# Optimization experiments

Hardware: AMD Instinct MI355X
Metric: run time of the kernel (lower is better)

## Reference

```python
import jax, jax.numpy as jnp
import numpy as np

B, S, D, K = 8, 4096, 256, 8192
BETA = 0.25


def setup_inputs() -> dict:
    key = jax.random.key(0)
    k1, k2 = jax.random.split(key)
    return {
        "z": jax.random.normal(k1, (B, S, D), dtype=jnp.float32),
        "embed": jax.random.normal(k2, (K, D), dtype=jnp.float32),
    }


def reference(z, embed):
    # Inference-path VQ-EMA forward (EMA buffer updates are a no-grad side
    # effect only active in training mode; excluded from the pure reference).
    num_codes, dim = embed.shape
    z_flat = z.reshape(-1, dim)                      # [N, D]
    # squared-euclidean distances: ||z||^2 - 2 z.e^T + ||e||^2  -> [N, K]
    dist = ((z_flat * z_flat).sum(1, keepdims=True)
            - 2.0 * (z_flat @ embed.T)
            + (embed * embed).sum(1)[None, :])
    idx = jnp.argmin(dist, axis=1)                   # [N]
    z_q = embed[idx].reshape(z.shape)                # gather instead of onehot @ embed
    # commitment loss: beta * mse(stop_grad(z_q), z)
    loss = BETA * jnp.mean(jnp.square(jax.lax.stop_gradient(z_q) - z))
    # straight-through estimator
    z_q_st = z + jax.lax.stop_gradient(z_q - z)
    # perplexity from code usage histogram (scatter-add instead of onehot.mean)
    counts = jnp.zeros((num_codes,), dtype=z.dtype).at[idx].add(1.0)
    avg_probs = counts / idx.shape[0]
    perplexity = jnp.exp(-jnp.sum(avg_probs * jnp.log(avg_probs + 1e-12)))
    return z_q_st, loss, perplexity, idx.reshape(z.shape[:-1])
```

## Files before the change

kernel.cpp:

```cpp
#include <hip/hip_runtime.h>
#include <stdint.h>
#include <math.h>

#define NROWS 32768
#define DIM   256
#define KCODES 8192
#define BETA  0.25f
#define RSPLIT 16
#define NELEM 8388608
#define TAU 0.09375f

typedef float f32x4 __attribute__((ext_vector_type(4)));
typedef _Float16 v8h __attribute__((ext_vector_type(8)));
typedef unsigned short us4 __attribute__((ext_vector_type(4)));

__device__ inline unsigned int split1(float x) {
    _Float16 hf = (_Float16)x;
    _Float16 lf = (_Float16)(x - (float)hf);
    unsigned int h = __builtin_bit_cast(unsigned short, hf);
    unsigned int l = __builtin_bit_cast(unsigned short, lf);
    return h | (l << 16);
}

__device__ inline void gload_lds16(const void* g, void* l) {
    __builtin_amdgcn_global_load_lds(
        (const __attribute__((address_space(1))) void*)g,
        (__attribute__((address_space(3))) void*)l,
        16, 0, 0);
}

__device__ inline unsigned int fkey(float f) {
    unsigned int b = __float_as_uint(f);
    return (b & 0x80000000u) ? ~b : (b | 0x80000000u);
}

__global__ void prep_all(const float* __restrict__ z,
                         const float* __restrict__ e,
                         unsigned short* __restrict__ zhi,
                         unsigned short* __restrict__ zlo,
                         unsigned short* __restrict__ ehi,
                         unsigned short* __restrict__ elo,
                         float* __restrict__ enrm,
                         float* __restrict__ counts,
                         float* __restrict__ lossAcc,
                         int* __restrict__ flagcnt) {
    if (blockIdx.x < 8192) {
        int t = blockIdx.x * 256 + threadIdx.x;
        float4 v = reinterpret_cast<const float4*>(z)[t];
        unsigned int p0 = split1(v.x);
        unsigned int p1 = split1(v.y);
        unsigned int p2 = split1(v.z);
        unsigned int p3 = split1(v.w);
        us4 h, l;
        h[0] = (unsigned short)p0; l[0] = (unsigned short)(p0 >> 16);
        h[1] = (unsigned short)p1; l[1] = (unsigned short)(p1 >> 16);
        h[2] = (unsigned short)p2; l[2] = (unsigned short)(p2 >> 16);
        h[3] = (unsigned short)p3; l[3] = (unsigned short)(p3 >> 16);
        reinterpret_cast<us4*>(zhi)[t] = h;
        reinterpret_cast<us4*>(zlo)[t] = l;
    } else {
        int row = blockIdx.x - 8192;
        int d = threadIdx.x;
        float x = e[(size_t)row * DIM + d];
        unsigned int p = split1(x);
        ehi[(size_t)row * DIM + d] = (unsigned short)p;
        elo[(size_t)row * DIM + d] = (unsigned short)(p >> 16);
        float sq = x * x;
        #pragma unroll
        for (int off = 32; off; off >>= 1) sq += __shfl_down(sq, off);
        __shared__ float ps[4];
        if ((threadIdx.x & 63) == 0) ps[threadIdx.x >> 6] = sq;
        __syncthreads();
        if (threadIdx.x == 0) {
            enrm[row] = 0.5f * (ps[0] + ps[1] + ps[2] + ps[3]);
            counts[row] = 0.f;
            if (row == 0) { *lossAcc = 0.f; *flagcnt = 0; }
        }
    }
}

__launch_bounds__(512, 2)
__global__ void gemm_hi_fused(const unsigned short* __restrict__ zhi,
                              const unsigned short* __restrict__ ehi,
                              const float* __restrict__ enrm,
                              int* __restrict__ colidx,
                              float* __restrict__ out_idx,
                              int* __restrict__ flagcnt,
                              int* __restrict__ flaglist,
                              unsigned long long* __restrict__ rkey) {
    __shared__ __align__(16) unsigned short Bs[4][128 * 128];
    __shared__ float rvv[4][128];
    __shared__ float rv2s[4][128];
    __shared__ int   rcc[4][128];

    const int tid = threadIdx.x;
    const int w = tid >> 6, l = tid & 63;
    const int lx = l & 15, quad = l >> 4;
    const int wm = w >> 2, wn = w & 3;
    const int arow_base = blockIdx.x * 128;
    const int fr_lx7 = lx & 7;
    const int ecol = wn * 32 + lx;

    const int st_row = w * 4 + (l >> 4);
    const int st_sw = ((l & 15) ^ (st_row & 7)) * 8;

    v8h af[4][8];
    #pragma unroll
    for (int mi = 0; mi < 4; ++mi) {
        const unsigned short* ap =
            zhi + (size_t)(arow_base + wm * 64 + mi * 16 + lx) * DIM + quad * 8;
        #pragma unroll
        for (int ks = 0; ks < 8; ++ks)
            af[mi][ks] = *(const v8h*)(ap + ks * 32);
    }

#define STAGE(BUF, CNT, KB) do {                                              \
        const unsigned short* _s = ehi                                        \
            + (((size_t)(CNT) * 128 + st_row) << 8) + (KB) * 128 + st_sw;     \
        unsigned short* _d = &Bs[BUF][(w * 4) * 128];                         \
        gload_lds16(_s,             _d);                                      \
        gload_lds16(_s + (32 << 8), _d + 32 * 128);                           \
        gload_lds16(_s + (64 << 8), _d + 64 * 128);                           \
        gload_lds16(_s + (96 << 8), _d + 96 * 128);                           \
} while (0)

#define FENCE_MFMA(BUF, BK) do {                                              \
        asm volatile("s_waitcnt vmcnt(14)" ::: "memory");                     \
        __builtin_amdgcn_s_barrier();                                         \
        asm volatile("" ::: "memory");                                        \
        __builtin_amdgcn_s_setprio(1);                                        \
        _Pragma("unroll") for (int kc = 0; kc < 4; ++kc) {                    \
            const int gsw = ((kc * 4 + quad) ^ fr_lx7) * 8;                   \
            v8h b0 = *(const v8h*)&Bs[BUF][(wn * 32 + lx) * 128 + gsw];       \
            v8h b1 = *(const v8h*)&Bs[BUF][(wn * 32 + 16 + lx) * 128 + gsw];  \
            _Pragma("unroll") for (int mi = 0; mi < 4; ++mi) {                \
                acc[mi][0] = __builtin_amdgcn_mfma_f32_16x16x32_f16(          \
                    af[mi][(BK) * 4 + kc], b0, acc[mi][0], 0, 0, 0);          \
                acc[mi][1] = __builtin_amdgcn_mfma_f32_16x16x32_f16(          \
                    af[mi][(BK) * 4 + kc], b1, acc[mi][1], 0, 0, 0);          \
            }                                                                 \
        }                                                                     \
        __builtin_amdgcn_s_setprio(0);                                        \
        asm volatile("" ::: "memory");                                        \
        __builtin_amdgcn_s_barrier();                                         \
} while (0)

#define EPILOGUE(NT) do {                                                     \
        _Pragma("unroll") for (int ni = 0; ni < 2; ++ni) {                    \
            const int col = (NT) * 128 + ecol + ni * 16;                      \
            _Pragma("unroll") for (int mi = 0; mi < 4; ++mi)                  \
                _Pragma("unroll") for (int r = 0; r < 4; ++r) {               \
                    const int s = mi * 4 + r;                                 \
                    const float a = acc[mi][ni][r];                           \
                    const bool gt = a > runm[s];                              \
                    runm2[s] = __builtin_amdgcn_fmed3f(a, runm[s], runm2[s]); \
                    runc[s] = gt ? col : runc[s];                             \
                    runm[s] = fmaxf(runm[s], a);                              \
                }                                                             \
        }                                                                     \
} while (0)

#define STEP_BK0(BUF, NT) do {                                                \
        const float a0 = -esn0, a1 = -esn1;                                   \
        _Pragma("unroll") for (int mi = 0; mi < 4; ++mi) {                    \
            acc[mi][0] = (f32x4){a0, a0, a0, a0};                             \
            acc[mi][1] = (f32x4){a1, a1, a1, a1};                             \
        }                                                                     \
        { const int nn = ((NT) + 1) & 63;                                     \
          esn0 = enrm[nn * 128 + ecol];                                       \
          esn1 = enrm[nn * 128 + ecol + 16]; }                                \
        STAGE((BUF + 3) & 3, ((NT) + 1) & 63, 1);                             \
        FENCE_MFMA(BUF, 0);                                                   \
} while (0)

#define STEP_BK1(BUF, NT) do {                                                \
        STAGE((BUF + 3) & 3, ((NT) + 2) & 63, 0);                             \
        FENCE_MFMA(BUF, 1);                                                   \
        EPILOGUE(NT);                                                         \
} while (0)

    float esn0 = enrm[ecol];
    float esn1 = enrm[ecol + 16];
    STAGE(0, 0, 0); STAGE(1, 0, 1); STAGE(2, 1, 0);

    float runm[16], runm2[16];
    int runc[16];
    #pragma unroll
    for (int s = 0; s < 16; ++s) {
        runm[s] = -3.0e38f; runm2[s] = -3.0e38f; runc[s] = 0x7fffffff;
    }

    f32x4 acc[4][2];
    for (int nt2 = 0; nt2 < 32; ++nt2) {
        const int nt0 = nt2 * 2;
        STEP_BK0(0, nt0);
        STEP_BK1(1, nt0);
        STEP_BK0(2, nt0 + 1);
        STEP_BK1(3, nt0 + 1);
    }
#undef STAGE
#undef FENCE_MFMA
#undef EPILOGUE
#undef STEP_BK0
#undef STEP_BK1

    #pragma unroll
    for (int s = 0; s < 16; ++s) {
        float m1 = runm[s], m2 = runm2[s];
        int c1 = runc[s];
        #pragma unroll
        for (int m = 1; m < 16; m <<= 1) {
            float o1 = __shfl_xor(m1, m);
            int oc = __shfl_xor(c1, m);
            float o2 = __shfl_xor(m2, m);
            float mn = fminf(m1, o1);
            m2 = fmaxf(fmaxf(m2, o2), mn);
            bool take = (o1 > m1) || (o1 == m1 && oc < c1);
            m1 = take ? o1 : m1;
            c1 = take ? oc : c1;
        }
        if (lx == 0) {
            const int rl = wm * 64 + (s >> 2) * 16 + quad * 4 + (s & 3);
            rvv[wn][rl] = m1; rcc[wn][rl] = c1; rv2s[wn][rl] = m2;
        }
    }
    __syncthreads();
    if (tid < 128) {
        float m1 = rvv[0][tid], m2 = rv2s[0][tid];
        int c1 = rcc[0][tid];
        #pragma unroll
        for (int q = 1; q < 4; ++q) {
            float o1 = rvv[q][tid], o2 = rv2s[q][tid];
            int oc = rcc[q][tid];
            float mn = fminf(m1, o1);
            m2 = fmaxf(fmaxf(m2, o2), mn);
            bool take = (o1 > m1) || (o1 == m1 && oc < c1);
            m1 = take ? o1 : m1;
            c1 = take ? oc : c1;
        }
        const float v1 = -m1, v2 = -m2;
        const int row = arow_base + tid;
        out_idx[row] = (float)c1;
        if (v2 - v1 < TAU) {
            int slot = atomicAdd(flagcnt, 1);
            flaglist[slot] = row;
            rkey[slot] = ~0ull;
            colidx[row] = -(slot + 1);
        } else {
            colidx[row] = c1;
        }
    }
}

__launch_bounds__(256, 2)
__global__ void rescue_gemm(const unsigned short* __restrict__ zhi,
                            const unsigned short* __restrict__ zlo,
                            const unsigned short* __restrict__ ehi,
                            const unsigned short* __restrict__ elo,
                            const float* __restrict__ enrm,
                            const int* __restrict__ flagcnt,
                            const int* __restrict__ flaglist,
                            unsigned long long* __restrict__ rkey) {
    __shared__ __align__(16) unsigned short As[128 * 64];
    __shared__ __align__(16) unsigned short Bs[128 * 64];
    __shared__ float rv[2][128];
    __shared__ int   rc[2][128];

    const int count = *flagcnt;
    const int tid = threadIdx.x;
    const int w = tid >> 6, l = tid & 63;
    const int lx = l & 15, quad = l >> 4;
    const int wm = w >> 1, wn = w & 1;
    const int cs = blockIdx.y;
    const int cbase_cs = cs * (KCODES / RSPLIT);

    const int st_row8 = l >> 3;
    const int st_g = (((l & 7) ^ (l >> 3)) * 8);
    const int fr_lx7 = lx & 7;

    for (int tb = blockIdx.x * 128; tb < count; tb += 32 * 128) {
        int arowj[4];
        #pragma unroll
        for (int j = 0; j < 4; ++j) {
            int li = tb + w * 32 + j * 8 + st_row8;
            arowj[j] = (li < count) ? flaglist[li] : 0;
        }

        float runv[16];
        int runc[16];
        #pragma unroll
        for (int s = 0; s < 16; ++s) { runv[s] = 3.0e38f; runc[s] = 0x7fffffff; }

        for (int nt = 0; nt < (KCODES / RSPLIT) / 128; ++nt) {
            const int colbase = cbase_cs + nt * 128;
            f32x4 acc[4][4];
            #pragma unroll
            for (int mi = 0; mi < 4; ++mi)
                #pragma unroll
                for (int ni = 0; ni < 4; ++ni) {
                    f32x4 zz = {0.f, 0.f, 0.f, 0.f};
                    acc[mi][ni] = zz;
                }

            #pragma unroll
            for (int seg = 0; seg < 3; ++seg) {
                const unsigned short* za = (seg == 2) ? zlo : zhi;
                const unsigned short* eb = (seg == 1) ? elo : ehi;
                for (int bk = 0; bk < 4; ++bk) {
                    const int ao = bk * 64;
                    __syncthreads();
                    #pragma unroll
                    for (int j = 0; j < 4; ++j) {
                        const int r = w * 32 + j * 8 + st_row8;
                        gload_lds16(za + (size_t)arowj[j] * DIM + ao + st_g,
                                    &As[(w * 32 + j * 8) * 64]);
                        gload_lds16(eb + (size_t)(colbase + r) * DIM + ao + st_g,
                                    &Bs[(w * 32 + j * 8) * 64]);
                    }
                    __syncthreads();
                    #pragma unroll
                    for (int kc = 0; kc < 2; ++kc) {
                        const int gsw = ((kc * 4 + quad) ^ fr_lx7) * 8;
                        v8h af[4], bfr[4];
                        #pragma unroll
                        for (int mi = 0; mi < 4; ++mi)
                            af[mi] = *(const v8h*)&As[(wm * 64 + mi * 16 + lx) * 64 + gsw];
                        #pragma unroll
                        for (int ni = 0; ni < 4; ++ni)
                            bfr[ni] = *(const v8h*)&Bs[(wn * 64 + ni * 16 + lx) * 64 + gsw];
                        #pragma unroll
                        for (int mi = 0; mi < 4; ++mi)
                            #pragma unroll
                            for (int ni = 0; ni < 4; ++ni)
                                acc[mi][ni] = __builtin_amdgcn_mfma_f32_16x16x32_f16(
                                    af[mi], bfr[ni], acc[mi][ni], 0, 0, 0);
                    }
                }
            }

            #pragma unroll
            for (int ni = 0; ni < 4; ++ni) {
                const int col = colbase + wn * 64 + ni * 16 + lx;
                const float es = enrm[col];
                #pragma unroll
                for (int mi = 0; mi < 4; ++mi)
                    #pragma unroll
                    for (int r = 0; r < 4; ++r) {
                        float sv = es - acc[mi][ni][r];
                        const int s = mi * 4 + r;
                        if (sv < runv[s]) { runv[s] = sv; runc[s] = col; }
                    }
            }
        }

        #pragma unroll
        for (int s = 0; s < 16; ++s) {
            float v = runv[s]; int c = runc[s];
            #pragma unroll
            for (int m = 1; m < 16; m <<= 1) {
                float ov = __shfl_xor(v, m);
                int oc = __shfl_xor(c, m);
                if (ov < v || (ov == v && oc < c)) { v = ov; c = oc; }
            }
            if (lx == 0) {
                const int mi = s >> 2, r = s & 3;
                const int rl = wm * 64 + mi * 16 + quad * 4 + r;
                rv[wn][rl] = v; rc[wn][rl] = c;
            }
        }
        __syncthreads();
        if (tid < 128) {
            float v0 = rv[0][tid]; int c0 = rc[0][tid];
            float v1 = rv[1][tid]; int c1 = rc[1][tid];
            if (v1 < v0 || (v1 == v0 && c1 < c0)) { v0 = v1; c0 = c1; }
            const int li = tb + tid;
            if (li < count) {
                unsigned long long key =
                    ((unsigned long long)fkey(v0) << 32) | (unsigned int)c0;
                atomicMin(&rkey[li], key);
            }
        }
        __syncthreads();
    }
}

__global__ void fused_out(const int* __restrict__ colidx,
                          const unsigned long long* __restrict__ rkey,
                          const float* __restrict__ z,
                          const float* __restrict__ embed,
                          float* __restrict__ out_zq,
                          float* __restrict__ out_idx,
                          float* __restrict__ counts,
                          float* __restrict__ lossAcc) {
    __shared__ int cidx[16];
    const int tid = threadIdx.x;
    if (tid < 16) {
        const int row = blockIdx.x * 16 + tid;
        int c = colidx[row];
        if (c < 0) {
            c = (int)(unsigned int)(rkey[-c - 1] & 0x1FFFull);
            out_idx[row] = (float)c;
        }
        cidx[tid] = c;
        atomicAdd(&counts[c], 1.0f);
    }
    __syncthreads();
    const int d = tid;
    float ls = 0.f;
    #pragma unroll 4
    for (int i = 0; i < 16; ++i) {
        const int row = blockIdx.x * 16 + i;
        const int c = cidx[i];
        const float zv = z[(size_t)row * DIM + d];
        const float ev = embed[(size_t)c * DIM + d];
        const float diff = ev - zv;
        out_zq[(size_t)row * DIM + d] = zv + diff;
        ls += diff * diff;
    }
    #pragma unroll
    for (int off = 32; off; off >>= 1) ls += __shfl_down(ls, off);
    __shared__ float ps[4];
    if ((tid & 63) == 0) ps[tid >> 6] = ls;
    __syncthreads();
    if (tid == 0) atomicAdd(lossAcc, ps[0] + ps[1] + ps[2] + ps[3]);
}

__global__ void finalize(const float* __restrict__ counts,
                         const float* __restrict__ lossAcc,
                         float* __restrict__ out_loss,
                         float* __restrict__ out_perp) {
    float h = 0.f;
    for (int k = threadIdx.x; k < KCODES; k += 256) {
        float p = counts[k] * (1.0f / (float)NROWS);
        h += p * logf(p + 1e-12f);
    }
    #pragma unroll
    for (int off = 32; off; off >>= 1) h += __shfl_down(h, off);
    __shared__ float ps[4];
    if ((threadIdx.x & 63) == 0) ps[threadIdx.x >> 6] = h;
    __syncthreads();
    if (threadIdx.x == 0) {
        *out_perp = expf(-(ps[0] + ps[1] + ps[2] + ps[3]));
        *out_loss = BETA * lossAcc[0] / (float)NELEM;
    }
}

extern "C" void kernel_launch(void* const* d_in, const int* in_sizes, int n_in,
                              void* d_out, int out_size, void* d_ws, size_t ws_size,
                              hipStream_t stream) {
    const float* z = (const float*)d_in[0];
    const float* embed = (const float*)d_in[1];
    char* ws = (char*)d_ws;

    unsigned short* zhi = (unsigned short*)(ws + 0);
    unsigned short* zlo = (unsigned short*)(ws + 16777216);
    unsigned short* ehi = (unsigned short*)(ws + 33554432);
    unsigned short* elo = (unsigned short*)(ws + 37748736);
    float* enrm    = (float*)(ws + 41943040);
    int*   colidx  = (int*)  (ws + 43548672);
    float* counts  = (float*)(ws + 43679744);
    float* lossAcc = (float*)(ws + 43712512);
    int*   flagcnt = (int*)  (ws + 43712516);
    int*   flaglist = (int*) (ws + 43712520);
    unsigned long long* rkey = (unsigned long long*)(ws + 43843592);

    float* out = (float*)d_out;
    float* out_zq   = out;
    float* out_loss = out + 8388608;
    float* out_perp = out + 8388609;
    float* out_idx  = out + 8388610;

    prep_all<<<16384, 256, 0, stream>>>(z, embed, zhi, zlo, ehi, elo, enrm,
                                        counts, lossAcc, flagcnt);
    gemm_hi_fused<<<NROWS / 128, 512, 0, stream>>>(
        zhi, ehi, enrm, colidx, out_idx, flagcnt, flaglist, rkey);
    rescue_gemm<<<dim3(32, RSPLIT), 256, 0, stream>>>(
        zhi, zlo, ehi, elo, enrm, flagcnt, flaglist, rkey);
    fused_out<<<NROWS / 16, 256, 0, stream>>>(colidx, rkey, z, embed,
                                              out_zq, out_idx, counts, lossAcc);
    finalize<<<1, 256, 0, stream>>>(counts, lossAcc, out_loss, out_perp);
}
```

Baseline: 352.4 us.

## Pipeline codebook K-chunks with register double-buffered LDS fragments

Restructures the fused GEMM+argmin main loop to stage 64-wide K chunks into four smaller LDS buffers and prefetch B fragments into registers one stage ahead, so LDS reads overlap with MFMAs. The old version used one barrier per half tile. The new one uses a single barrier per quarter tile with a shallow vmcnt wait. Codebook norms are preloaded once into LDS instead of being read from global per tile. This adds 32KB of LDS for the norms, more barriers and more fragment registers, which could affect occupancy at 2 blocks per CU.

```diff
diff --git a/kernel.cpp b/kernel.cpp
--- a/kernel.cpp
+++ b/kernel.cpp
@@ -88,7 +88,8 @@
                               int* __restrict__ flagcnt,
                               int* __restrict__ flaglist,
                               unsigned long long* __restrict__ rkey) {
-    __shared__ __align__(16) unsigned short Bs[4][128 * 128];
+    __shared__ __align__(16) unsigned short Bs[4][128 * 64];
+    __shared__ float esL[KCODES];
     __shared__ float rvv[4][128];
     __shared__ float rv2s[4][128];
     __shared__ int   rcc[4][128];
@@ -98,11 +99,9 @@
     const int lx = l & 15, quad = l >> 4;
     const int wm = w >> 2, wn = w & 3;
     const int arow_base = blockIdx.x * 128;
-    const int fr_lx7 = lx & 7;
+    const int fr_lx7 = lx & 15 & 7;
     const int ecol = wn * 32 + lx;
-
-    const int st_row = w * 4 + (l >> 4);
-    const int st_sw = ((l & 15) ^ (st_row & 7)) * 8;
+    const int st_g = ((l & 7) ^ (l >> 3)) * 8;
 
     v8h af[4][8];
     #pragma unroll
@@ -114,40 +113,46 @@
             af[mi][ks] = *(const v8h*)(ap + ks * 32);
     }
 
-#define STAGE(BUF, CNT, KB) do {                                              \
+    #pragma unroll
+    for (int j = 0; j < 4; ++j)
+        gload_lds16(enrm + (j * 8 + w) * 256 + l * 4, &esL[(j * 8 + w) * 256]);
+
+#define STAGE(BUF, NT, BK) do {                                               \
         const unsigned short* _s = ehi                                        \
-            + (((size_t)(CNT) * 128 + st_row) << 8) + (KB) * 128 + st_sw;     \
-        unsigned short* _d = &Bs[BUF][(w * 4) * 128];                         \
-        gload_lds16(_s,             _d);                                      \
-        gload_lds16(_s + (32 << 8), _d + 32 * 128);                           \
-        gload_lds16(_s + (64 << 8), _d + 64 * 128);                           \
-        gload_lds16(_s + (96 << 8), _d + 96 * 128);                           \
+            + (size_t)((NT) * 128 + (tid >> 3)) * DIM + (BK) * 64 + st_g;     \
+        gload_lds16(_s,                    &Bs[BUF][(w * 8) * 64]);           \
+        gload_lds16(_s + (size_t)64 * DIM, &Bs[BUF][(64 + w * 8) * 64]);      \
 } while (0)
 
-#define FENCE_MFMA(BUF, BK) do {                                              \
-        asm volatile("s_waitcnt vmcnt(14)" ::: "memory");                     \
+#define READF(DST, BUF) do {                                                  \
+        _Pragma("unroll") for (int kc = 0; kc < 2; ++kc) {                    \
+            const int gsw = ((kc * 4 + quad) ^ fr_lx7) * 8;                   \
+            DST[kc * 2 + 0] = *(const v8h*)&Bs[BUF][(wn * 32 + lx) * 64 + gsw];      \
+            DST[kc * 2 + 1] = *(const v8h*)&Bs[BUF][(wn * 32 + 16 + lx) * 64 + gsw]; \
+        }                                                                     \
+} while (0)
+
+#define MFMAS(F, BK) do {                                                     \
+        __builtin_amdgcn_s_setprio(1);                                        \
+        _Pragma("unroll") for (int kc = 0; kc < 2; ++kc)                      \
+            _Pragma("unroll") for (int mi = 0; mi < 4; ++mi) {                \
+                acc[mi][0] = __builtin_amdgcn_mfma_f32_16x16x32_f16(          \
+                    af[mi][(BK) * 2 + kc], F[kc * 2 + 0], acc[mi][0], 0, 0, 0); \
+                acc[mi][1] = __builtin_amdgcn_mfma_f32_16x16x32_f16(          \
+                    af[mi][(BK) * 2 + kc], F[kc * 2 + 1], acc[mi][1], 0, 0, 0); \
+            }                                                                 \
+        __builtin_amdgcn_s_setprio(0);                                        \
+} while (0)
+
+#define FENCE2 do {                                                           \
+        asm volatile("s_waitcnt vmcnt(2)" ::: "memory");                      \
         __builtin_amdgcn_s_barrier();                                         \
         asm volatile("" ::: "memory");                                        \
-        __builtin_amdgcn_s_setprio(1);                                        \
-        _Pragma("unroll") for (int kc = 0; kc < 4; ++kc) {                    \
-            const int gsw = ((kc * 4 + quad) ^ fr_lx7) * 8;                   \
-            v8h b0 = *(const v8h*)&Bs[BUF][(wn * 32 + lx) * 128 + gsw];       \
-            v8h b1 = *(const v8h*)&Bs[BUF][(wn * 32 + 16 + lx) * 128 + gsw];  \
-            _Pragma("unroll") for (int mi = 0; mi < 4; ++mi) {                \
-                acc[mi][0] = __builtin_amdgcn_mfma_f32_16x16x32_f16(          \
-                    af[mi][(BK) * 4 + kc], b0, acc[mi][0], 0, 0, 0);          \
-                acc[mi][1] = __builtin_amdgcn_mfma_f32_16x16x32_f16(          \
-                    af[mi][(BK) * 4 + kc], b1, acc[mi][1], 0, 0, 0);          \
-            }                                                                 \
-        }                                                                     \
-        __builtin_amdgcn_s_setprio(0);                                        \
-        asm volatile("" ::: "memory");                                        \
-        __builtin_amdgcn_s_barrier();                                         \
 } while (0)
 
-#define EPILOGUE(NT) do {                                                     \
+#define EPILOGUE(NTV) do {                                                    \
         _Pragma("unroll") for (int ni = 0; ni < 2; ++ni) {                    \
-            const int col = (NT) * 128 + ecol + ni * 16;                      \
+            const int col = (NTV) * 128 + ecol + ni * 16;                     \
             _Pragma("unroll") for (int mi = 0; mi < 4; ++mi)                  \
                 _Pragma("unroll") for (int r = 0; r < 4; ++r) {               \
                     const int s = mi * 4 + r;                                 \
@@ -160,28 +165,13 @@
         }                                                                     \
 } while (0)
 
-#define STEP_BK0(BUF, NT) do {                                                \
-        const float a0 = -esn0, a1 = -esn1;                                   \
-        _Pragma("unroll") for (int mi = 0; mi < 4; ++mi) {                    \
-            acc[mi][0] = (f32x4){a0, a0, a0, a0};                             \
-            acc[mi][1] = (f32x4){a1, a1, a1, a1};                             \
-        }                                                                     \
-        { const int nn = ((NT) + 1) & 63;                                     \
-          esn0 = enrm[nn * 128 + ecol];                                       \
-          esn1 = enrm[nn * 128 + ecol + 16]; }                                \
-        STAGE((BUF + 3) & 3, ((NT) + 1) & 63, 1);                             \
-        FENCE_MFMA(BUF, 0);                                                   \
-} while (0)
-
-#define STEP_BK1(BUF, NT) do {                                                \
-        STAGE((BUF + 3) & 3, ((NT) + 2) & 63, 0);                             \
-        FENCE_MFMA(BUF, 1);                                                   \
-        EPILOGUE(NT);                                                         \
-} while (0)
-
-    float esn0 = enrm[ecol];
-    float esn1 = enrm[ecol + 16];
-    STAGE(0, 0, 0); STAGE(1, 0, 1); STAGE(2, 1, 0);
+    STAGE(0, 0, 0);
+    STAGE(1, 0, 1);
+    v8h bA[4], bB[4];
+    FENCE2;
+    READF(bA, 0);
+    float esn0 = esL[ecol];
+    float esn1 = esL[ecol + 16];
 
     float runm[16], runm2[16];
     int runc[16];
@@ -191,18 +181,40 @@
     }
 
     f32x4 acc[4][2];
-    for (int nt2 = 0; nt2 < 32; ++nt2) {
-        const int nt0 = nt2 * 2;
-        STEP_BK0(0, nt0);
-        STEP_BK1(1, nt0);
-        STEP_BK0(2, nt0 + 1);
-        STEP_BK1(3, nt0 + 1);
+    for (int nt = 0; nt < 64; ++nt) {
+        const int ntn = (nt + 1) & 63;
+        STAGE(2, nt, 2);
+        FENCE2;
+        {   const float a0 = -esn0, a1 = -esn1;
+            #pragma unroll
+            for (int mi = 0; mi < 4; ++mi) {
+                acc[mi][0] = (f32x4){a0, a0, a0, a0};
+                acc[mi][1] = (f32x4){a1, a1, a1, a1};
+            }
+        }
+        READF(bB, 1);
+        MFMAS(bA, 0);
+        STAGE(3, nt, 3);
+        FENCE2;
+        READF(bA, 2);
+        MFMAS(bB, 1);
+        STAGE(0, ntn, 0);
+        FENCE2;
+        READF(bB, 3);
+        MFMAS(bA, 2);
+        STAGE(1, ntn, 1);
+        FENCE2;
+        READF(bA, 0);
+        esn0 = esL[ntn * 128 + ecol];
+        esn1 = esL[ntn * 128 + ecol + 16];
+        MFMAS(bB, 3);
+        EPILOGUE(nt);
     }
 #undef STAGE
-#undef FENCE_MFMA
+#undef READF
+#undef MFMAS
+#undef FENCE2
 #undef EPILOGUE
-#undef STEP_BK0
-#undef STEP_BK1
 
     #pragma unroll
     for (int s = 0; s < 16; ++s) {
```

New measurement: 354.1 us. Within noise of the previous version (+0.5%).
